# Kernel optimization log

Measured on AMD Instinct MI355X. Metric: run time of the kernel, lower is better.

## Reference

```python
import jax, jax.numpy as jnp
import numpy as np

B, S, F = 8, 4096, 512
H, A, L, DK = 8, 512, 64, 33  # n_head, n_attn, n_landmarks, d_kernel
D = A // H  # d_k = 64


def setup_inputs() -> dict:
    key = jax.random.key(0)
    ks = jax.random.split(key, 12)
    s = 0.02
    return {
        "query": jax.random.normal(ks[0], (B, S, F), jnp.float32),
        "key": jax.random.normal(ks[1], (B, S, F), jnp.float32),
        "value": jax.random.normal(ks[2], (B, S, F), jnp.float32),
        "mask": jnp.ones((B, 1, S), jnp.bool_),
        "Wq": jax.random.normal(ks[3], (F, A), jnp.float32) * s,
        "bq": jnp.zeros((A,), jnp.float32),
        "Wk": jax.random.normal(ks[4], (F, A), jnp.float32) * s,
        "bk": jnp.zeros((A,), jnp.float32),
        "Wv": jax.random.normal(ks[5], (F, A), jnp.float32) * s,
        "bv": jnp.zeros((A,), jnp.float32),
        "Wo": jax.random.normal(ks[6], (A, F), jnp.float32) * s,
        "bo": jnp.zeros((F,), jnp.float32),
        "conv_w": jax.random.normal(ks[7], (H, 1, DK, 1), jnp.float32) * s,
    }


def iterative_inv(mat, n_iter=6):
    # mat: [B, H, L, L]
    I = jnp.eye(mat.shape[-1], dtype=mat.dtype)
    K = mat
    denom = jnp.max(jnp.sum(K, axis=-2), axis=-1)[:, :, None, None]
    V = jnp.swapaxes(K, -1, -2) / denom
    for _ in range(n_iter):
        KV = K @ V
        V = 0.25 * V @ (13 * I - KV @ (15 * I - KV @ (7 * I - KV)))
    return V


def reference(query, key, value, mask, Wq, bq, Wk, bk, Wv, bv, Wo, bo, conv_w):
    nb, seq, _ = query.shape
    q = (query @ Wq + bq).reshape(nb, seq, H, D).transpose(0, 2, 1, 3)  # [B,H,S,D]
    k = (key @ Wk + bk).reshape(nb, seq, H, D).transpose(0, 2, 1, 3)
    v = (value @ Wv + bv).reshape(nb, seq, H, D).transpose(0, 2, 1, 3)
    scale = D ** -0.25
    q = q * scale
    k = k * scale
    m = seq // L + 1  # segment length per landmark
    q_rep = jnp.concatenate([q, q, q], axis=2)[:, :, : m * L, :]
    k_rep = jnp.concatenate([k, k, k], axis=2)[:, :, : m * L, :]
    q_land = q_rep.reshape(nb, H, L, m, D).mean(axis=3)  # [B,H,L,D]
    k_land = k_rep.reshape(nb, H, L, m, D).mean(axis=3)
    ker1 = jax.nn.softmax(jnp.einsum("bhsd,bhld->bhsl", q, k_land), axis=-1)
    ker2 = jax.nn.softmax(jnp.einsum("bhld,bhmd->bhlm", q_land, k_land), axis=-1)
    ker3 = jax.nn.softmax(jnp.einsum("bhld,bhsd->bhls", q_land, k), axis=-1)
    x = ker1 @ (iterative_inv(ker2) @ (ker3 @ v))  # [B,H,S,D]
    # depthwise conv over the sequence axis (kernel (DK,1), groups=H)
    pad = DK // 2
    conv_out = jax.lax.conv_general_dilated(
        v, conv_w, window_strides=(1, 1), padding=((pad, pad), (0, 0)),
        feature_group_count=H, dimension_numbers=("NCHW", "OIHW", "NCHW"))
    x = x + conv_out
    x = x.transpose(0, 2, 1, 3).reshape(nb, seq, H * D)
    return x @ Wo + bo
```

## Files before the change

kernel.cpp:

```cpp
#include <hip/hip_runtime.h>
#include <hip/hip_bf16.h>
#include <hip/hip_fp16.h>

#define SEQ 4096
#define NBATCH 8
#define NHEAD 8
#define DKW 33
#define LDP 68

typedef _Float16 f16x8 __attribute__((ext_vector_type(8)));
typedef _Float16 f16x4 __attribute__((ext_vector_type(4)));
typedef float f32x4 __attribute__((ext_vector_type(4)));

__global__ __launch_bounds__(256) void cvt_w4_k(
    const float* __restrict__ Wq, const float* __restrict__ Wk,
    const float* __restrict__ Wv, const float* __restrict__ Wo,
    _Float16* __restrict__ WtBase, float scl)
{
  __shared__ float T[64][65];
  int z = blockIdx.z;
  const float* W = (z == 0) ? Wq : (z == 1) ? Wk : (z == 2) ? Wv : Wo;
  float scale = (z < 2) ? scl : 1.0f;
  _Float16* Wt = WtBase + (size_t)z * 262144;
  int n0 = blockIdx.x * 64, k0 = blockIdx.y * 64;
  int tid = threadIdx.x;
#pragma unroll
  for (int i = 0; i < 16; i++) {
    int e = i * 256 + tid; int r = e >> 6, c = e & 63;
    T[r][c] = W[(size_t)(k0 + r) * 512 + n0 + c];
  }
  __syncthreads();
#pragma unroll
  for (int i = 0; i < 16; i++) {
    int e = i * 256 + tid; int r = e >> 6, c = e & 63;
    Wt[(size_t)(n0 + r) * 512 + k0 + c] = (_Float16)(T[c][r] * scale);
  }
}

__device__ __forceinline__ void gl_lds16(const void* g, _Float16* l) {
  __builtin_amdgcn_global_load_lds(
      (const __attribute__((address_space(1))) void*)g,
      (__attribute__((address_space(3))) void*)l, 16, 0, 0);
}

__global__ __launch_bounds__(512, 2) void gemm_bp3_k(
    const float* __restrict__ A0, const float* __restrict__ A1, const float* __restrict__ A2,
    const _Float16* __restrict__ WtBase,
    const float* __restrict__ b0, const float* __restrict__ b1, const float* __restrict__ b2,
    float scl, _Float16* __restrict__ qh, _Float16* __restrict__ kh, _Float16* __restrict__ vt)
{
  __shared__ __attribute__((aligned(16))) _Float16 Bl[128 * 516];
  const int z = blockIdx.z;
  const float* A = (z == 0) ? A0 : (z == 1) ? A1 : A2;
  const _Float16* Wt = WtBase + (size_t)z * 262144;
  const float* bias = (z == 0) ? b0 : (z == 1) ? b1 : b2;
  const float bscale = (z < 2) ? scl : 1.0f;
  const int tid = threadIdx.x;
  const int lane = tid & 63, wv = tid >> 6;
  const int l15 = lane & 15, l4 = lane >> 4;
  const int col0 = blockIdx.y * 128;
  const int row0 = blockIdx.x * 512;

  {
    int n = tid >> 2, kc = (tid & 3) * 128;
    const _Float16* wp = &Wt[(size_t)(col0 + n) * 512 + kc];
    _Float16* lp = &Bl[n * 516 + kc];
#pragma unroll
    for (int i = 0; i < 16; i++)
      *(f16x8*)&lp[i * 8] = *(const f16x8*)&wp[i * 8];
  }

  size_t abase[4];
#pragma unroll
  for (int mt = 0; mt < 4; mt++)
    abase[mt] = (size_t)(row0 + wv * 64 + mt * 16 + l15) * 512;

  auto loadA = [&](int mt, int ks) -> f16x8 {
    int k = ks * 32 + l4 * 8;
    float4 x = *(const float4*)&A[abase[mt] + k];
    float4 y = *(const float4*)&A[abase[mt] + k + 4];
    f16x8 o;
    o[0] = (_Float16)x.x; o[1] = (_Float16)x.y; o[2] = (_Float16)x.z; o[3] = (_Float16)x.w;
    o[4] = (_Float16)y.x; o[5] = (_Float16)y.y; o[6] = (_Float16)y.z; o[7] = (_Float16)y.w;
    return o;
  };

  f32x4 acc[4][8];
#pragma unroll
  for (int mt = 0; mt < 4; mt++)
#pragma unroll
    for (int n = 0; n < 8; n++) acc[mt][n] = (f32x4){0.f, 0.f, 0.f, 0.f};

  f16x8 aC[4];
#pragma unroll
  for (int mt = 0; mt < 4; mt++) aC[mt] = loadA(mt, 0);
  __syncthreads();

  for (int ks = 0; ks < 16; ks++) {
    f16x8 aN[4];
    if (ks < 15) {
#pragma unroll
      for (int mt = 0; mt < 4; mt++) aN[mt] = loadA(mt, ks + 1);
    }
    f16x8 bf[8];
#pragma unroll
    for (int n = 0; n < 8; n++)
      bf[n] = *(const f16x8*)&Bl[(n * 16 + l15) * 516 + ks * 32 + l4 * 8];
    __builtin_amdgcn_s_setprio(1);
#pragma unroll
    for (int mt = 0; mt < 4; mt++)
#pragma unroll
      for (int n = 0; n < 8; n++)
        acc[mt][n] = __builtin_amdgcn_mfma_f32_16x16x32_f16(aC[mt], bf[n], acc[mt][n], 0, 0, 0);
    __builtin_amdgcn_s_setprio(0);
    if (ks < 15) {
#pragma unroll
      for (int mt = 0; mt < 4; mt++) aC[mt] = aN[mt];
    }
  }

  float bb[8];
#pragma unroll
  for (int n = 0; n < 8; n++) bb[n] = bias[col0 + n * 16 + l15] * bscale;

  if (z == 2) {
    __syncthreads();
#pragma unroll
    for (int mt = 0; mt < 4; mt++)
#pragma unroll
      for (int n = 0; n < 8; n++) {
        f16x4 o;
#pragma unroll
        for (int r = 0; r < 4; r++) o[r] = (_Float16)(acc[mt][n][r] + bb[n]);
        *(f16x4*)&Bl[(n * 16 + l15) * 516 + wv * 64 + mt * 16 + l4 * 4] = o;
      }
    __syncthreads();
    int b = row0 >> 12, sbase = row0 & 4095;
#pragma unroll
    for (int i = 0; i < 16; i++) {
      int idx = i * 512 + tid;
      int c = idx >> 6, sc = (idx & 63) * 8;
      int colg_ = col0 + c;
      int h = colg_ >> 6, d = colg_ & 63;
      f16x8 v = *(const f16x8*)&Bl[c * 516 + sc];
      *(f16x8*)&vt[((size_t)((b * NHEAD + h) * 64 + d)) * SEQ + sbase + sc] = v;
    }
  } else {
    _Float16* outp = (z == 0) ? qh : kh;
#pragma unroll
    for (int mt = 0; mt < 4; mt++) {
      int rb = row0 + wv * 64 + mt * 16 + l4 * 4;
#pragma unroll
      for (int n = 0; n < 8; n++) {
        int col = col0 + n * 16 + l15;
        int h = col >> 6, d = col & 63;
#pragma unroll
        for (int r = 0; r < 4; r++) {
          int row = rb + r;
          int b = row >> 12, s = row & 4095;
          outp[((size_t)(b * NHEAD + h) * SEQ + s) * 64 + d] = (_Float16)(acc[mt][n][r] + bb[n]);
        }
      }
    }
  }
}

__global__ __launch_bounds__(256, 4) void gemm_gl_k(
    const _Float16* __restrict__ A, const _Float16* __restrict__ Wt,
    const float* __restrict__ bias, float* __restrict__ outp)
{
  __shared__ __attribute__((aligned(16))) _Float16 smem[16384];
  const int tid = threadIdx.x;
  const int lane = tid & 63, wv = tid >> 6;
  const int wr = wv >> 1, wc = wv & 1;
  const int l15 = lane & 15, l4 = lane >> 4;
  const int row0 = blockIdx.x * 128, col0 = blockIdx.y * 128;

  auto stage = [&](int buf, int ks) {
#pragma unroll
    for (int c = 0; c < 2; c++) {
      int u = wv * 128 + c * 64 + lane;
      int r = u & 127, s = u >> 7;
      int grow = row0 + r;
      size_t ga = ((size_t)((grow >> 12) * NHEAD + (ks >> 1)) * SEQ + (grow & 4095)) * 64
                  + (ks & 1) * 32 + s * 8;
      size_t gb = (size_t)(col0 + r) * 512 + ks * 32 + s * 8;
      int dst = (wv * 128 + c * 64) * 8;
      gl_lds16(&A[ga],  &smem[buf * 4096 + dst]);
      gl_lds16(&Wt[gb], &smem[8192 + buf * 4096 + dst]);
    }
  };

  f32x4 acc[4][4];
#pragma unroll
  for (int m = 0; m < 4; m++)
#pragma unroll
    for (int n = 0; n < 4; n++) acc[m][n] = (f32x4){0.f, 0.f, 0.f, 0.f};

  stage(0, 0);
  __syncthreads();

  for (int ks = 0; ks < 16; ks++) {
    const int cur = ks & 1;
    if (ks < 15) stage(cur ^ 1, ks + 1);
    const int ao = cur * 4096, bo = 8192 + cur * 4096;
    f16x8 af[4], bf[4];
#pragma unroll
    for (int m = 0; m < 4; m++)
      af[m] = *(const f16x8*)&smem[ao + l4 * 1024 + (wr * 64 + m * 16 + l15) * 8];
#pragma unroll
    for (int n = 0; n < 4; n++)
      bf[n] = *(const f16x8*)&smem[bo + l4 * 1024 + (wc * 64 + n * 16 + l15) * 8];
#pragma unroll
    for (int m = 0; m < 4; m++)
#pragma unroll
      for (int n = 0; n < 4; n++)
        acc[m][n] = __builtin_amdgcn_mfma_f32_16x16x32_f16(af[m], bf[n], acc[m][n], 0, 0, 0);
    __syncthreads();
  }

  float bb[4];
#pragma unroll
  for (int n = 0; n < 4; n++) bb[n] = bias[col0 + wc * 64 + n * 16 + l15];
#pragma unroll
  for (int mt = 0; mt < 4; mt++) {
    int rb = row0 + wr * 64 + mt * 16 + l4 * 4;
#pragma unroll
    for (int n = 0; n < 4; n++) {
      int col = col0 + wc * 64 + n * 16 + l15;
#pragma unroll
      for (int r = 0; r < 4; r++)
        outp[(size_t)(rb + r) * 512 + col] = acc[mt][n][r] + bb[n];
    }
  }
}

__global__ void landmarks_k(const _Float16* __restrict__ q, const _Float16* __restrict__ k,
                            float* __restrict__ qlandf, float* __restrict__ klandf,
                            _Float16* __restrict__ ql16, _Float16* __restrict__ kl16)
{
  int bhl = blockIdx.x;
  int d = threadIdx.x;
  int l = bhl & 63, bh = bhl >> 6;
  const _Float16* qp = q + (size_t)bh * SEQ * 64;
  const _Float16* kp = k + (size_t)bh * SEQ * 64;
  float sq = 0.f, sk = 0.f;
  int base = l * 65;
  for (int i = 0; i < 65; i++) {
    int s = (base + i) & 4095;
    sq += (float)qp[(size_t)s * 64 + d];
    sk += (float)kp[(size_t)s * 64 + d];
  }
  float mq = sq * (1.0f / 65.0f), mk = sk * (1.0f / 65.0f);
  qlandf[(size_t)bhl * 64 + d] = mq;
  klandf[(size_t)bhl * 64 + d] = mk;
  ql16[(size_t)bhl * 64 + d] = (_Float16)mq;
  kl16[(size_t)bhl * 64 + d] = (_Float16)mk;
}

__device__ __forceinline__ void mfma64(
    float (&C)[64][LDP], const float (&X)[64][LDP], const float (&Yt)[64][LDP],
    int wv, int l15, int l4)
{
  f16x8 ah[2], al[2];
#pragma unroll
  for (int kh = 0; kh < 2; kh++) {
    const float* xp = &X[wv * 16 + l15][kh * 32 + l4 * 8];
    float4 x0 = *(const float4*)xp;
    float4 x1 = *(const float4*)(xp + 4);
    float xv[8] = {x0.x, x0.y, x0.z, x0.w, x1.x, x1.y, x1.z, x1.w};
#pragma unroll
    for (int j = 0; j < 8; j++) {
      _Float16 h = (_Float16)xv[j];
      ah[kh][j] = h;
      al[kh][j] = (_Float16)(xv[j] - (float)h);
    }
  }
  f32x4 acc[4];
#pragma unroll
  for (int n = 0; n < 4; n++) {
    f16x8 bh_[2], bl_[2];
#pragma unroll
    for (int kh = 0; kh < 2; kh++) {
      const float* yp = &Yt[n * 16 + l15][kh * 32 + l4 * 8];
      float4 y0 = *(const float4*)yp;
      float4 y1 = *(const float4*)(yp + 4);
      float yv[8] = {y0.x, y0.y, y0.z, y0.w, y1.x, y1.y, y1.z, y1.w};
#pragma unroll
      for (int j = 0; j < 8; j++) {
        _Float16 h = (_Float16)yv[j];
        bh_[kh][j] = h;
        bl_[kh][j] = (_Float16)(yv[j] - (float)h);
      }
    }
    acc[n] = (f32x4){0.f, 0.f, 0.f, 0.f};
#pragma unroll
    for (int kh = 0; kh < 2; kh++) {
      acc[n] = __builtin_amdgcn_mfma_f32_16x16x32_f16(ah[kh], bh_[kh], acc[n], 0, 0, 0);
      acc[n] = __builtin_amdgcn_mfma_f32_16x16x32_f16(ah[kh], bl_[kh], acc[n], 0, 0, 0);
      acc[n] = __builtin_amdgcn_mfma_f32_16x16x32_f16(al[kh], bh_[kh], acc[n], 0, 0, 0);
    }
  }
#pragma unroll
  for (int n = 0; n < 4; n++)
#pragma unroll
    for (int r = 0; r < 4; r++)
      C[wv * 16 + l4 * 4 + r][n * 16 + l15] = acc[n][r];
  __syncthreads();
}

__global__ __launch_bounds__(256) void ker2_inv_k(
    const float* __restrict__ qland, const float* __restrict__ kland, float* __restrict__ invm)
{
  __shared__ float Km[64][LDP], Vm[64][LDP], VmT[64][LDP], KV[64][LDP], T1t[64][LDP], T2[64][LDP];
  __shared__ float colsum[64];
  __shared__ float denom_s;
  int bh = blockIdx.x, tid = threadIdx.x;
  int lane = tid & 63, wv = tid >> 6, l15 = lane & 15, l4 = lane >> 4;
  const float* qlp = qland + (size_t)bh * 4096;
  const float* klp = kland + (size_t)bh * 4096;
  const int r = tid >> 2, cq = (tid & 3) * 16;
#pragma unroll
  for (int j = 0; j < 4; j++) {
    *(float4*)&T2[r][cq + j * 4]  = *(const float4*)&qlp[(size_t)r * 64 + cq + j * 4];
    *(float4*)&T1t[r][cq + j * 4] = *(const float4*)&klp[(size_t)r * 64 + cq + j * 4];
  }
  __syncthreads();
  mfma64(Km, T2, T1t, wv, l15, l4);
  {
    float4 v[4];
#pragma unroll
    for (int j = 0; j < 4; j++) v[j] = *(const float4*)&Km[r][cq + j * 4];
    float mx = -1e30f;
#pragma unroll
    for (int j = 0; j < 4; j++) mx = fmaxf(mx, fmaxf(fmaxf(v[j].x, v[j].y), fmaxf(v[j].z, v[j].w)));
    mx = fmaxf(mx, __shfl_xor(mx, 1));
    mx = fmaxf(mx, __shfl_xor(mx, 2));
    float s = 0.f;
#pragma unroll
    for (int j = 0; j < 4; j++) {
      v[j].x = __expf(v[j].x - mx); v[j].y = __expf(v[j].y - mx);
      v[j].z = __expf(v[j].z - mx); v[j].w = __expf(v[j].w - mx);
      s += v[j].x + v[j].y + v[j].z + v[j].w;
    }
    s += __shfl_xor(s, 1);
    s += __shfl_xor(s, 2);
    float iv = 1.0f / s;
#pragma unroll
    for (int j = 0; j < 4; j++) {
      v[j].x *= iv; v[j].y *= iv; v[j].z *= iv; v[j].w *= iv;
      *(float4*)&Km[r][cq + j * 4] = v[j];
    }
  }
  __syncthreads();
  {
    float s = 0.f;
#pragma unroll
    for (int i = 0; i < 16; i++) s += Km[cq + i][r];
    s += __shfl_xor(s, 1);
    s += __shfl_xor(s, 2);
    if ((tid & 3) == 0) colsum[r] = s;
  }
  __syncthreads();
  if (tid < 64) {
    float v = colsum[tid];
#pragma unroll
    for (int off = 1; off < 64; off <<= 1) v = fmaxf(v, __shfl_xor(v, off));
    if (tid == 0) denom_s = v;
  }
  __syncthreads();
  {
    float dn = 1.0f / denom_s;
#pragma unroll
    for (int j = 0; j < 4; j++) {
      float4 v = *(const float4*)&Km[r][cq + j * 4];
      v.x *= dn; v.y *= dn; v.z *= dn; v.w *= dn;
      *(float4*)&VmT[r][cq + j * 4] = v;
      Vm[cq + j * 4 + 0][r] = v.x;
      Vm[cq + j * 4 + 1][r] = v.y;
      Vm[cq + j * 4 + 2][r] = v.z;
      Vm[cq + j * 4 + 3][r] = v.w;
    }
  }
  __syncthreads();
  for (int it = 0; it < 6; it++) {
    mfma64(KV, Km, VmT, wv, l15, l4);
#pragma unroll
    for (int j = 0; j < 4; j++) {
      float4 v = *(const float4*)&KV[r][cq + j * 4];
#pragma unroll
      for (int e = 0; e < 4; e++) {
        int col = cq + j * 4 + e;
        T1t[col][r] = (r == col ? 7.0f : 0.0f) - ((const float*)&v)[e];
      }
    }
    __syncthreads();
    mfma64(T2, KV, T1t, wv, l15, l4);
#pragma unroll
    for (int j = 0; j < 4; j++) {
      float4 v = *(const float4*)&T2[r][cq + j * 4];
#pragma unroll
      for (int e = 0; e < 4; e++) {
        int col = cq + j * 4 + e;
        T1t[col][r] = (r == col ? 15.0f : 0.0f) - ((const float*)&v)[e];
      }
    }
    __syncthreads();
    mfma64(T2, KV, T1t, wv, l15, l4);
#pragma unroll
    for (int j = 0; j < 4; j++) {
      float4 v = *(const float4*)&T2[r][cq + j * 4];
#pragma unroll
      for (int e = 0; e < 4; e++) {
        int col = cq + j * 4 + e;
        T1t[col][r] = (r == col ? 13.0f : 0.0f) - ((const float*)&v)[e];
      }
    }
    __syncthreads();
    mfma64(T2, Vm, T1t, wv, l15, l4);
#pragma unroll
    for (int j = 0; j < 4; j++) {
      float4 v = *(const float4*)&T2[r][cq + j * 4];
      v.x *= 0.25f; v.y *= 0.25f; v.z *= 0.25f; v.w *= 0.25f;
      *(float4*)&Vm[r][cq + j * 4] = v;
      VmT[cq + j * 4 + 0][r] = v.x;
      VmT[cq + j * 4 + 1][r] = v.y;
      VmT[cq + j * 4 + 2][r] = v.z;
      VmT[cq + j * 4 + 3][r] = v.w;
    }
    __syncthreads();
  }
#pragma unroll
  for (int j = 0; j < 4; j++)
    *(float4*)&invm[(size_t)bh * 4096 + (size_t)r * 64 + cq + j * 4] = *(const float4*)&Vm[r][cq + j * 4];
}

__global__ __launch_bounds__(256) void ker3pv_k(
    const _Float16* __restrict__ kx, const _Float16* __restrict__ vt,
    const _Float16* __restrict__ ql16,
    float* __restrict__ t1part, float* __restrict__ csumpart)
{
  __shared__ __attribute__((aligned(16))) _Float16 kls[64 * 72];
  __shared__ __attribute__((aligned(16))) _Float16 vls[64 * 72];
  __shared__ __attribute__((aligned(16))) _Float16 pls[64 * 72];
  __shared__ float red[4][64];
  int g = blockIdx.x, bh = blockIdx.y;
  int tid = threadIdx.x, lane = tid & 63, wv = tid >> 6;
  const _Float16* kp = kx + (size_t)bh * SEQ * 64;
  const _Float16* vp = vt + (size_t)bh * 64 * SEQ;
  const _Float16* qlp = ql16 + (size_t)bh * 4096;
  const int l15 = lane & 15, l4 = lane >> 4;

  f16x8 qa[4][2];
#pragma unroll
  for (int lt = 0; lt < 4; lt++)
#pragma unroll
    for (int kh = 0; kh < 2; kh++)
      qa[lt][kh] = *(const f16x8*)&qlp[(size_t)(lt * 16 + l15) * 64 + kh * 32 + l4 * 8];

  float cs[16];
#pragma unroll
  for (int i = 0; i < 16; i++) cs[i] = 0.f;
  f32x4 accp[4];
#pragma unroll
  for (int lt = 0; lt < 4; lt++) accp[lt] = (f32x4){0.f, 0.f, 0.f, 0.f};

  const int srow = tid >> 2, c4 = tid & 3;
  for (int t = 0; t < 16; t++) {
    int s0 = g * 1024 + t * 64;
    __syncthreads();
    *(f16x8*)&kls[srow * 72 + c4 * 8]       = *(const f16x8*)&kp[(size_t)(s0 + srow) * 64 + c4 * 8];
    *(f16x8*)&kls[srow * 72 + (c4 + 4) * 8] = *(const f16x8*)&kp[(size_t)(s0 + srow) * 64 + (c4 + 4) * 8];
    *(f16x8*)&vls[srow * 72 + c4 * 8]       = *(const f16x8*)&vp[(size_t)srow * SEQ + s0 + c4 * 8];
    *(f16x8*)&vls[srow * 72 + (c4 + 4) * 8] = *(const f16x8*)&vp[(size_t)srow * SEQ + s0 + (c4 + 4) * 8];
    __syncthreads();
    f16x8 kb[2];
    kb[0] = *(const f16x8*)&kls[(wv * 16 + l15) * 72 + l4 * 8];
    kb[1] = *(const f16x8*)&kls[(wv * 16 + l15) * 72 + 32 + l4 * 8];
    f32x4 C[4];
#pragma unroll
    for (int lt = 0; lt < 4; lt++) {
      C[lt] = (f32x4){0.f, 0.f, 0.f, 0.f};
      C[lt] = __builtin_amdgcn_mfma_f32_16x16x32_f16(qa[lt][0], kb[0], C[lt], 0, 0, 0);
      C[lt] = __builtin_amdgcn_mfma_f32_16x16x32_f16(qa[lt][1], kb[1], C[lt], 0, 0, 0);
    }
#pragma unroll
    for (int lt = 0; lt < 4; lt++)
#pragma unroll
      for (int r = 0; r < 4; r++) {
        float e = __expf(C[lt][r]);
        cs[lt * 4 + r] += e;
        pls[(lt * 16 + l4 * 4 + r) * 72 + wv * 16 + l15] = (_Float16)e;
      }
    __syncthreads();
    f16x8 va[2];
    va[0] = *(const f16x8*)&vls[(wv * 16 + l15) * 72 + l4 * 8];
    va[1] = *(const f16x8*)&vls[(wv * 16 + l15) * 72 + 32 + l4 * 8];
#pragma unroll
    for (int lt = 0; lt < 4; lt++) {
      f16x8 pb0 = *(const f16x8*)&pls[(lt * 16 + l15) * 72 + l4 * 8];
      f16x8 pb1 = *(const f16x8*)&pls[(lt * 16 + l15) * 72 + 32 + l4 * 8];
      accp[lt] = __builtin_amdgcn_mfma_f32_16x16x32_f16(va[0], pb0, accp[lt], 0, 0, 0);
      accp[lt] = __builtin_amdgcn_mfma_f32_16x16x32_f16(va[1], pb1, accp[lt], 0, 0, 0);
    }
  }
  size_t pbase = ((size_t)(bh * 4 + g)) * 4096;
#pragma unroll
  for (int lt = 0; lt < 4; lt++)
#pragma unroll
    for (int r = 0; r < 4; r++)
      t1part[pbase + (size_t)(wv * 16 + l4 * 4 + r) * 64 + lt * 16 + l15] = accp[lt][r];
#pragma unroll
  for (int i = 0; i < 16; i++) {
    cs[i] += __shfl_xor(cs[i], 1);
    cs[i] += __shfl_xor(cs[i], 2);
    cs[i] += __shfl_xor(cs[i], 4);
    cs[i] += __shfl_xor(cs[i], 8);
  }
  if (l15 == 0) {
#pragma unroll
    for (int lt = 0; lt < 4; lt++)
#pragma unroll
      for (int r = 0; r < 4; r++)
        red[wv][lt * 16 + l4 * 4 + r] = cs[lt * 4 + r];
  }
  __syncthreads();
  if (tid < 64)
    csumpart[((size_t)(bh * 4 + g)) * 64 + tid] = red[0][tid] + red[1][tid] + red[2][tid] + red[3][tid];
}

__global__ void t1_reduce_k(const float* __restrict__ t1part, const float* __restrict__ csumpart,
                            float* __restrict__ t1r)
{
  int i = blockIdx.x * 256 + threadIdx.x;
  int bh = i >> 12, dl = i & 4095, l = dl & 63;
  float s = 0.f, cssum = 0.f;
#pragma unroll
  for (int g = 0; g < 4; g++) {
    s += t1part[(((size_t)(bh * 4 + g)) << 12) + dl];
    cssum += csumpart[(((size_t)(bh * 4 + g)) << 6) + l];
  }
  t1r[i] = s / cssum;
}

__global__ __launch_bounds__(256) void t2_mm_k(
    const float* __restrict__ invm, const float* __restrict__ t1r, _Float16* __restrict__ t2t)
{
  __shared__ float T[64][68];
  __shared__ float I[64][68];
  int bh = blockIdx.x;
  int tid = threadIdx.x;
  const float* ip = invm + (size_t)bh * 4096;
  const float* tp = t1r + (size_t)bh * 4096;
  int r = tid >> 2;
#pragma unroll
  for (int mq = 0; mq < 4; mq++) {
    int d0 = (tid & 3) * 16 + mq * 4;
    *(float4*)&T[r][d0] = *(const float4*)&tp[(size_t)r * 64 + d0];
    *(float4*)&I[r][d0] = *(const float4*)&ip[(size_t)r * 64 + d0];
  }
  __syncthreads();
  int ty = tid >> 4, tx = tid & 15;
  float acc[4][4] = {};
#pragma unroll 4
  for (int kk = 0; kk < 64; kk++) {
    float a_[4], b_[4];
#pragma unroll
    for (int i = 0; i < 4; i++) a_[i] = T[ty * 4 + i][kk];
#pragma unroll
    for (int j = 0; j < 4; j++) b_[j] = I[tx * 4 + j][kk];
#pragma unroll
    for (int i = 0; i < 4; i++)
#pragma unroll
      for (int j = 0; j < 4; j++)
        acc[i][j] = fmaf(a_[i], b_[j], acc[i][j]);
  }
#pragma unroll
  for (int i = 0; i < 4; i++) {
    f16x4 o;
    o[0] = (_Float16)acc[i][0]; o[1] = (_Float16)acc[i][1];
    o[2] = (_Float16)acc[i][2]; o[3] = (_Float16)acc[i][3];
    *(f16x4*)&t2t[(size_t)bh * 4096 + (size_t)(ty * 4 + i) * 64 + tx * 4] = o;
  }
}

__global__ __launch_bounds__(256) void x1conv_k(
    const _Float16* __restrict__ qx, const _Float16* __restrict__ kl16,
    const _Float16* __restrict__ t2t, const _Float16* __restrict__ vt,
    const float* __restrict__ cw, _Float16* __restrict__ xq)
{
  __shared__ __attribute__((aligned(16))) _Float16 qls[64 * 72];
  __shared__ __attribute__((aligned(16))) _Float16 t2ls[64 * 72];
  __shared__ __attribute__((aligned(16))) _Float16 pls[64 * 72];
  __shared__ __attribute__((aligned(16))) _Float16 vls[64 * 98];
  int c = blockIdx.x, bh = blockIdx.y;
  int s0 = c * 64;
  int tid = threadIdx.x, lane = tid & 63, wv = tid >> 6;
  const int l15 = lane & 15, l4 = lane >> 4;
  const int h = bh & 7;
  const _Float16* qp = qx + ((size_t)bh * SEQ + s0) * 64;
  const int srow = tid >> 2, c4 = tid & 3;
  *(f16x8*)&qls[srow * 72 + c4 * 8]       = *(const f16x8*)&qp[(size_t)srow * 64 + c4 * 8];
  *(f16x8*)&qls[srow * 72 + (c4 + 4) * 8] = *(const f16x8*)&qp[(size_t)srow * 64 + (c4 + 4) * 8];
  *(f16x8*)&t2ls[srow * 72 + c4 * 8]       = *(const f16x8*)&t2t[(size_t)bh * 4096 + (size_t)srow * 64 + c4 * 8];
  *(f16x8*)&t2ls[srow * 72 + (c4 + 4) * 8] = *(const f16x8*)&t2t[(size_t)bh * 4096 + (size_t)srow * 64 + (c4 + 4) * 8];
  {
    const _Float16* vp = vt + ((size_t)bh * 64 + srow) * SEQ;
    int base = s0 - 16 + c4 * 24;
#pragma unroll
    for (int i = 0; i < 3; i++) {
      int s = base + i * 8;
      f16x8 v;
      if (s >= 0 && s + 8 <= SEQ) {
        v = *(const f16x8*)&vp[s];
      } else {
#pragma unroll
        for (int j = 0; j < 8; j++) {
          int sj = s + j;
          v[j] = (sj >= 0 && sj < SEQ) ? vp[sj] : (_Float16)0.f;
        }
      }
      *(f16x8*)&vls[srow * 98 + c4 * 24 + i * 8] = v;
    }
  }
  float w[DKW];
#pragma unroll
  for (int j = 0; j < DKW; j++) w[j] = cw[h * DKW + j];
  f16x8 klb[4][2];
#pragma unroll
  for (int lt = 0; lt < 4; lt++)
#pragma unroll
    for (int kh = 0; kh < 2; kh++)
      klb[lt][kh] = *(const f16x8*)&kl16[(size_t)bh * 4096 + (size_t)(lt * 16 + l15) * 64 + kh * 32 + l4 * 8];
  __syncthreads();
  f16x8 qaf[2];
  qaf[0] = *(const f16x8*)&qls[(wv * 16 + l15) * 72 + l4 * 8];
  qaf[1] = *(const f16x8*)&qls[(wv * 16 + l15) * 72 + 32 + l4 * 8];
  f32x4 C[4];
#pragma unroll
  for (int lt = 0; lt < 4; lt++) {
    C[lt] = (f32x4){0.f, 0.f, 0.f, 0.f};
    C[lt] = __builtin_amdgcn_mfma_f32_16x16x32_f16(qaf[0], klb[lt][0], C[lt], 0, 0, 0);
    C[lt] = __builtin_amdgcn_mfma_f32_16x16x32_f16(qaf[1], klb[lt][1], C[lt], 0, 0, 0);
  }
  float e[16], rs[4];
#pragma unroll
  for (int r = 0; r < 4; r++) rs[r] = 0.f;
#pragma unroll
  for (int lt = 0; lt < 4; lt++)
#pragma unroll
    for (int r = 0; r < 4; r++) {
      e[lt * 4 + r] = __expf(C[lt][r]);
      rs[r] += e[lt * 4 + r];
    }
#pragma unroll
  for (int r = 0; r < 4; r++) {
    rs[r] += __shfl_xor(rs[r], 1);
    rs[r] += __shfl_xor(rs[r], 2);
    rs[r] += __shfl_xor(rs[r], 4);
    rs[r] += __shfl_xor(rs[r], 8);
    rs[r] = 1.0f / rs[r];
  }
#pragma unroll
  for (int lt = 0; lt < 4; lt++)
#pragma unroll
    for (int r = 0; r < 4; r++)
      pls[(wv * 16 + l4 * 4 + r) * 72 + lt * 16 + l15] = (_Float16)(e[lt * 4 + r] * rs[r]);
  __syncthreads();
  f16x8 pa[2];
  pa[0] = *(const f16x8*)&pls[(wv * 16 + l15) * 72 + l4 * 8];
  pa[1] = *(const f16x8*)&pls[(wv * 16 + l15) * 72 + 32 + l4 * 8];
  __syncthreads();
  {
    int d = tid & 63, sg = tid >> 6;
    float win[48];
#pragma unroll
    for (int t = 0; t < 48; t++) win[t] = (float)vls[d * 98 + sg * 16 + t];
#pragma unroll
    for (int i = 0; i < 16; i++) {
      float a = 0.f;
#pragma unroll
      for (int j = 0; j < DKW; j++) a = fmaf(w[j], win[i + j], a);
      pls[(sg * 16 + i) * 72 + d] = (_Float16)a;
    }
  }
  __syncthreads();
#pragma unroll
  for (int dt = 0; dt < 4; dt++) {
    f16x8 tb0 = *(const f16x8*)&t2ls[(dt * 16 + l15) * 72 + l4 * 8];
    f16x8 tb1 = *(const f16x8*)&t2ls[(dt * 16 + l15) * 72 + 32 + l4 * 8];
    f32x4 X = (f32x4){0.f, 0.f, 0.f, 0.f};
    X = __builtin_amdgcn_mfma_f32_16x16x32_f16(pa[0], tb0, X, 0, 0, 0);
    X = __builtin_amdgcn_mfma_f32_16x16x32_f16(pa[1], tb1, X, 0, 0, 0);
#pragma unroll
    for (int r = 0; r < 4; r++) {
      int sl = wv * 16 + l4 * 4 + r;
      int d = dt * 16 + l15;
      float vvv = X[r] + (float)pls[sl * 72 + d];
      xq[((size_t)bh * SEQ + s0 + sl) * 64 + d] = (_Float16)vvv;
    }
  }
}

extern "C" void kernel_launch(void* const* d_in, const int* in_sizes, int n_in,
                              void* d_out, int out_size, void* d_ws, size_t ws_size,
                              hipStream_t stream)
{
  (void)in_sizes; (void)n_in; (void)out_size; (void)ws_size;
  const float* query = (const float*)d_in[0];
  const float* key_  = (const float*)d_in[1];
  const float* value = (const float*)d_in[2];
  const float* Wq = (const float*)d_in[4];
  const float* bq = (const float*)d_in[5];
  const float* Wk = (const float*)d_in[6];
  const float* bk = (const float*)d_in[7];
  const float* Wv = (const float*)d_in[8];
  const float* bv = (const float*)d_in[9];
  const float* Wo = (const float*)d_in[10];
  const float* bo = (const float*)d_in[11];
  const float* cw = (const float*)d_in[12];
  float* out = (float*)d_out;

  const size_t NQ = (size_t)NBATCH * NHEAD * SEQ * 64;
  _Float16* qh  = (_Float16*)d_ws;
  _Float16* kh  = qh + NQ;
  _Float16* vt  = kh + NQ;
  _Float16* WtB = vt + NQ;
  _Float16* WoT = WtB + 3 * 262144;
  _Float16* ql16 = WtB + 4 * 262144;
  _Float16* kl16 = ql16 + 262144;
  _Float16* t2t  = kl16 + 262144;
  float* qlandf = (float*)(t2t + 262144);
  float* klandf = qlandf + 262144;
  float* invb   = klandf + 262144;
  float* t1r    = invb + 262144;
  float* t1part = t1r + 262144;
  float* csumpart = t1part + 4 * 262144;

  const float scl = 0.3535533905932738f;

  cvt_w4_k<<<dim3(8, 8, 4), 256, 0, stream>>>(Wq, Wk, Wv, Wo, WtB, scl);

  gemm_bp3_k<<<dim3(64, 4, 3), 512, 0, stream>>>(query, key_, value, WtB,
                                                 bq, bk, bv, scl, qh, kh, vt);

  landmarks_k<<<4096, 64, 0, stream>>>(qh, kh, qlandf, klandf, ql16, kl16);
  ker2_inv_k<<<64, 256, 0, stream>>>(qlandf, klandf, invb);
  ker3pv_k<<<dim3(4, 64), 256, 0, stream>>>(kh, vt, ql16, t1part, csumpart);
  t1_reduce_k<<<1024, 256, 0, stream>>>(t1part, csumpart, t1r);
  t2_mm_k<<<64, 256, 0, stream>>>(invb, t1r, t2t);
  x1conv_k<<<dim3(64, 64), 256, 0, stream>>>(qh, kl16, t2t, vt, cw, qh);
  gemm_gl_k<<<dim3(256, 4), 256, 0, stream>>>(qh, WoT, bo, out);
}
```

Measured before the change: 295.1 us.

## Merge iterative inverse and ker3·V into one launch, fold reduction into t2

Combines the independent ker2 iterative-inverse kernel (64 blocks) and the ker3·V partial kernel (256 blocks) into one 320-block launch. Blocks pick their role from the block index and share one static shared-memory buffer. The separate t1 reduce kernel is removed, and t2_mm_k now sums the four partials and applies the column-sum normalization itself. The aim is to cut two launches and let the serial inverse run alongside the streaming work. The cost is that every block reserves about 104 KB of shared memory, which can limit how many ker3 blocks are resident per CU.

Result: faster. 273.3 us (-7.4%).

```diff
diff --git a/kernel.cpp b/kernel.cpp
--- a/kernel.cpp
+++ b/kernel.cpp
@@ -259,7 +259,7 @@
 }
 
 __device__ __forceinline__ void mfma64(
-    float (&C)[64][LDP], const float (&X)[64][LDP], const float (&Yt)[64][LDP],
+    float (*C)[LDP], const float (*X)[LDP], const float (*Yt)[LDP],
     int wv, int l15, int l4)
 {
   f16x8 ah[2], al[2];
@@ -309,254 +309,264 @@
   __syncthreads();
 }
 
-__global__ __launch_bounds__(256) void ker2_inv_k(
-    const float* __restrict__ qland, const float* __restrict__ kland, float* __restrict__ invm)
-{
-  __shared__ float Km[64][LDP], Vm[64][LDP], VmT[64][LDP], KV[64][LDP], T1t[64][LDP], T2[64][LDP];
-  __shared__ float colsum[64];
-  __shared__ float denom_s;
-  int bh = blockIdx.x, tid = threadIdx.x;
-  int lane = tid & 63, wv = tid >> 6, l15 = lane & 15, l4 = lane >> 4;
-  const float* qlp = qland + (size_t)bh * 4096;
-  const float* klp = kland + (size_t)bh * 4096;
-  const int r = tid >> 2, cq = (tid & 3) * 16;
-#pragma unroll
-  for (int j = 0; j < 4; j++) {
-    *(float4*)&T2[r][cq + j * 4]  = *(const float4*)&qlp[(size_t)r * 64 + cq + j * 4];
-    *(float4*)&T1t[r][cq + j * 4] = *(const float4*)&klp[(size_t)r * 64 + cq + j * 4];
-  }
-  __syncthreads();
-  mfma64(Km, T2, T1t, wv, l15, l4);
-  {
-    float4 v[4];
-#pragma unroll
-    for (int j = 0; j < 4; j++) v[j] = *(const float4*)&Km[r][cq + j * 4];
-    float mx = -1e30f;
-#pragma unroll
-    for (int j = 0; j < 4; j++) mx = fmaxf(mx, fmaxf(fmaxf(v[j].x, v[j].y), fmaxf(v[j].z, v[j].w)));
-    mx = fmaxf(mx, __shfl_xor(mx, 1));
-    mx = fmaxf(mx, __shfl_xor(mx, 2));
-    float s = 0.f;
-#pragma unroll
-    for (int j = 0; j < 4; j++) {
-      v[j].x = __expf(v[j].x - mx); v[j].y = __expf(v[j].y - mx);
-      v[j].z = __expf(v[j].z - mx); v[j].w = __expf(v[j].w - mx);
-      s += v[j].x + v[j].y + v[j].z + v[j].w;
-    }
-    s += __shfl_xor(s, 1);
-    s += __shfl_xor(s, 2);
-    float iv = 1.0f / s;
-#pragma unroll
-    for (int j = 0; j < 4; j++) {
-      v[j].x *= iv; v[j].y *= iv; v[j].z *= iv; v[j].w *= iv;
-      *(float4*)&Km[r][cq + j * 4] = v[j];
-    }
-  }
-  __syncthreads();
-  {
-    float s = 0.f;
-#pragma unroll
-    for (int i = 0; i < 16; i++) s += Km[cq + i][r];
-    s += __shfl_xor(s, 1);
-    s += __shfl_xor(s, 2);
-    if ((tid & 3) == 0) colsum[r] = s;
-  }
-  __syncthreads();
-  if (tid < 64) {
-    float v = colsum[tid];
-#pragma unroll
-    for (int off = 1; off < 64; off <<= 1) v = fmaxf(v, __shfl_xor(v, off));
-    if (tid == 0) denom_s = v;
-  }
-  __syncthreads();
-  {
-    float dn = 1.0f / denom_s;
-#pragma unroll
-    for (int j = 0; j < 4; j++) {
-      float4 v = *(const float4*)&Km[r][cq + j * 4];
-      v.x *= dn; v.y *= dn; v.z *= dn; v.w *= dn;
-      *(float4*)&VmT[r][cq + j * 4] = v;
-      Vm[cq + j * 4 + 0][r] = v.x;
-      Vm[cq + j * 4 + 1][r] = v.y;
-      Vm[cq + j * 4 + 2][r] = v.z;
-      Vm[cq + j * 4 + 3][r] = v.w;
-    }
-  }
-  __syncthreads();
-  for (int it = 0; it < 6; it++) {
-    mfma64(KV, Km, VmT, wv, l15, l4);
-#pragma unroll
-    for (int j = 0; j < 4; j++) {
-      float4 v = *(const float4*)&KV[r][cq + j * 4];
-#pragma unroll
-      for (int e = 0; e < 4; e++) {
-        int col = cq + j * 4 + e;
-        T1t[col][r] = (r == col ? 7.0f : 0.0f) - ((const float*)&v)[e];
-      }
-    }
-    __syncthreads();
-    mfma64(T2, KV, T1t, wv, l15, l4);
-#pragma unroll
-    for (int j = 0; j < 4; j++) {
-      float4 v = *(const float4*)&T2[r][cq + j * 4];
-#pragma unroll
-      for (int e = 0; e < 4; e++) {
-        int col = cq + j * 4 + e;
-        T1t[col][r] = (r == col ? 15.0f : 0.0f) - ((const float*)&v)[e];
-      }
-    }
-    __syncthreads();
-    mfma64(T2, KV, T1t, wv, l15, l4);
-#pragma unroll
-    for (int j = 0; j < 4; j++) {
-      float4 v = *(const float4*)&T2[r][cq + j * 4];
-#pragma unroll
-      for (int e = 0; e < 4; e++) {
-        int col = cq + j * 4 + e;
-        T1t[col][r] = (r == col ? 13.0f : 0.0f) - ((const float*)&v)[e];
-      }
-    }
-    __syncthreads();
-    mfma64(T2, Vm, T1t, wv, l15, l4);
-#pragma unroll
-    for (int j = 0; j < 4; j++) {
-      float4 v = *(const float4*)&T2[r][cq + j * 4];
-      v.x *= 0.25f; v.y *= 0.25f; v.z *= 0.25f; v.w *= 0.25f;
-      *(float4*)&Vm[r][cq + j * 4] = v;
-      VmT[cq + j * 4 + 0][r] = v.x;
-      VmT[cq + j * 4 + 1][r] = v.y;
-      VmT[cq + j * 4 + 2][r] = v.z;
-      VmT[cq + j * 4 + 3][r] = v.w;
-    }
-    __syncthreads();
-  }
-#pragma unroll
-  for (int j = 0; j < 4; j++)
-    *(float4*)&invm[(size_t)bh * 4096 + (size_t)r * 64 + cq + j * 4] = *(const float4*)&Vm[r][cq + j * 4];
-}
-
-__global__ __launch_bounds__(256) void ker3pv_k(
+#define SMEM_BYTES 104712
+
+__global__ __launch_bounds__(256) void attn_mid_k(
+    const float* __restrict__ qland, const float* __restrict__ kland,
     const _Float16* __restrict__ kx, const _Float16* __restrict__ vt,
     const _Float16* __restrict__ ql16,
-    float* __restrict__ t1part, float* __restrict__ csumpart)
-{
-  __shared__ __attribute__((aligned(16))) _Float16 kls[64 * 72];
-  __shared__ __attribute__((aligned(16))) _Float16 vls[64 * 72];
-  __shared__ __attribute__((aligned(16))) _Float16 pls[64 * 72];
-  __shared__ float red[4][64];
-  int g = blockIdx.x, bh = blockIdx.y;
-  int tid = threadIdx.x, lane = tid & 63, wv = tid >> 6;
-  const _Float16* kp = kx + (size_t)bh * SEQ * 64;
-  const _Float16* vp = vt + (size_t)bh * 64 * SEQ;
-  const _Float16* qlp = ql16 + (size_t)bh * 4096;
+    float* __restrict__ invm, float* __restrict__ t1part, float* __restrict__ csumpart)
+{
+  __shared__ __attribute__((aligned(16))) char smem[SMEM_BYTES];
+  const int bid = blockIdx.x;
+  const int tid = threadIdx.x;
+  const int lane = tid & 63, wv = tid >> 6;
   const int l15 = lane & 15, l4 = lane >> 4;
 
-  f16x8 qa[4][2];
-#pragma unroll
-  for (int lt = 0; lt < 4; lt++)
-#pragma unroll
-    for (int kh = 0; kh < 2; kh++)
-      qa[lt][kh] = *(const f16x8*)&qlp[(size_t)(lt * 16 + l15) * 64 + kh * 32 + l4 * 8];
-
-  float cs[16];
-#pragma unroll
-  for (int i = 0; i < 16; i++) cs[i] = 0.f;
-  f32x4 accp[4];
-#pragma unroll
-  for (int lt = 0; lt < 4; lt++) accp[lt] = (f32x4){0.f, 0.f, 0.f, 0.f};
-
-  const int srow = tid >> 2, c4 = tid & 3;
-  for (int t = 0; t < 16; t++) {
-    int s0 = g * 1024 + t * 64;
-    __syncthreads();
-    *(f16x8*)&kls[srow * 72 + c4 * 8]       = *(const f16x8*)&kp[(size_t)(s0 + srow) * 64 + c4 * 8];
-    *(f16x8*)&kls[srow * 72 + (c4 + 4) * 8] = *(const f16x8*)&kp[(size_t)(s0 + srow) * 64 + (c4 + 4) * 8];
-    *(f16x8*)&vls[srow * 72 + c4 * 8]       = *(const f16x8*)&vp[(size_t)srow * SEQ + s0 + c4 * 8];
-    *(f16x8*)&vls[srow * 72 + (c4 + 4) * 8] = *(const f16x8*)&vp[(size_t)srow * SEQ + s0 + (c4 + 4) * 8];
-    __syncthreads();
-    f16x8 kb[2];
-    kb[0] = *(const f16x8*)&kls[(wv * 16 + l15) * 72 + l4 * 8];
-    kb[1] = *(const f16x8*)&kls[(wv * 16 + l15) * 72 + 32 + l4 * 8];
-    f32x4 C[4];
-#pragma unroll
-    for (int lt = 0; lt < 4; lt++) {
-      C[lt] = (f32x4){0.f, 0.f, 0.f, 0.f};
-      C[lt] = __builtin_amdgcn_mfma_f32_16x16x32_f16(qa[lt][0], kb[0], C[lt], 0, 0, 0);
-      C[lt] = __builtin_amdgcn_mfma_f32_16x16x32_f16(qa[lt][1], kb[1], C[lt], 0, 0, 0);
-    }
+  if (bid < 64) {
+    float (*Km)[LDP]  = (float (*)[LDP])(smem);
+    float (*Vm)[LDP]  = (float (*)[LDP])(smem + 17408);
+    float (*VmT)[LDP] = (float (*)[LDP])(smem + 2 * 17408);
+    float (*KV)[LDP]  = (float (*)[LDP])(smem + 3 * 17408);
+    float (*T1t)[LDP] = (float (*)[LDP])(smem + 4 * 17408);
+    float (*T2)[LDP]  = (float (*)[LDP])(smem + 5 * 17408);
+    float* colsum = (float*)(smem + 6 * 17408);
+    const int bh = bid;
+    const float* qlp = qland + (size_t)bh * 4096;
+    const float* klp = kland + (size_t)bh * 4096;
+    const int r = tid >> 2, cq = (tid & 3) * 16;
+#pragma unroll
+    for (int j = 0; j < 4; j++) {
+      *(float4*)&T2[r][cq + j * 4]  = *(const float4*)&qlp[(size_t)r * 64 + cq + j * 4];
+      *(float4*)&T1t[r][cq + j * 4] = *(const float4*)&klp[(size_t)r * 64 + cq + j * 4];
+    }
+    __syncthreads();
+    mfma64(Km, T2, T1t, wv, l15, l4);
+    {
+      float4 v[4];
+#pragma unroll
+      for (int j = 0; j < 4; j++) v[j] = *(const float4*)&Km[r][cq + j * 4];
+      float mx = -1e30f;
+#pragma unroll
+      for (int j = 0; j < 4; j++) mx = fmaxf(mx, fmaxf(fmaxf(v[j].x, v[j].y), fmaxf(v[j].z, v[j].w)));
+      mx = fmaxf(mx, __shfl_xor(mx, 1));
+      mx = fmaxf(mx, __shfl_xor(mx, 2));
+      float s = 0.f;
+#pragma unroll
+      for (int j = 0; j < 4; j++) {
+        v[j].x = __expf(v[j].x - mx); v[j].y = __expf(v[j].y - mx);
+        v[j].z = __expf(v[j].z - mx); v[j].w = __expf(v[j].w - mx);
+        s += v[j].x + v[j].y + v[j].z + v[j].w;
+      }
+      s += __shfl_xor(s, 1);
+      s += __shfl_xor(s, 2);
+      float iv = 1.0f / s;
+#pragma unroll
+      for (int j = 0; j < 4; j++) {
+        v[j].x *= iv; v[j].y *= iv; v[j].z *= iv; v[j].w *= iv;
+        *(float4*)&Km[r][cq + j * 4] = v[j];
+      }
+    }
+    __syncthreads();
+    {
+      float s = 0.f;
+#pragma unroll
+      for (int i = 0; i < 16; i++) s += Km[cq + i][r];
+      s += __shfl_xor(s, 1);
+      s += __shfl_xor(s, 2);
+      if ((tid & 3) == 0) colsum[r] = s;
+    }
+    __syncthreads();
+    if (tid < 64) {
+      float v = colsum[tid];
+#pragma unroll
+      for (int off = 1; off < 64; off <<= 1) v = fmaxf(v, __shfl_xor(v, off));
+      if (tid == 0) colsum[64] = v;
+    }
+    __syncthreads();
+    {
+      float dn = 1.0f / colsum[64];
+#pragma unroll
+      for (int j = 0; j < 4; j++) {
+        float4 v = *(const float4*)&Km[r][cq + j * 4];
+        v.x *= dn; v.y *= dn; v.z *= dn; v.w *= dn;
+        *(float4*)&VmT[r][cq + j * 4] = v;
+        Vm[cq + j * 4 + 0][r] = v.x;
+        Vm[cq + j * 4 + 1][r] = v.y;
+        Vm[cq + j * 4 + 2][r] = v.z;
+        Vm[cq + j * 4 + 3][r] = v.w;
+      }
+    }
+    __syncthreads();
+    for (int it = 0; it < 6; it++) {
+      mfma64(KV, Km, VmT, wv, l15, l4);
+#pragma unroll
+      for (int j = 0; j < 4; j++) {
+        float4 v = *(const float4*)&KV[r][cq + j * 4];
+#pragma unroll
+        for (int e = 0; e < 4; e++) {
+          int col = cq + j * 4 + e;
+          T1t[col][r] = (r == col ? 7.0f : 0.0f) - ((const float*)&v)[e];
+        }
+      }
+      __syncthreads();
+      mfma64(T2, KV, T1t, wv, l15, l4);
+#pragma unroll
+      for (int j = 0; j < 4; j++) {
+        float4 v = *(const float4*)&T2[r][cq + j * 4];
+#pragma unroll
+        for (int e = 0; e < 4; e++) {
+          int col = cq + j * 4 + e;
+          T1t[col][r] = (r == col ? 15.0f : 0.0f) - ((const float*)&v)[e];
+        }
+      }
+      __syncthreads();
+      mfma64(T2, KV, T1t, wv, l15, l4);
+#pragma unroll
+      for (int j = 0; j < 4; j++) {
+        float4 v = *(const float4*)&T2[r][cq + j * 4];
+#pragma unroll
+        for (int e = 0; e < 4; e++) {
+          int col = cq + j * 4 + e;
+          T1t[col][r] = (r == col ? 13.0f : 0.0f) - ((const float*)&v)[e];
+        }
+      }
+      __syncthreads();
+      mfma64(T2, Vm, T1t, wv, l15, l4);
+#pragma unroll
+      for (int j = 0; j < 4; j++) {
+        float4 v = *(const float4*)&T2[r][cq + j * 4];
+        v.x *= 0.25f; v.y *= 0.25f; v.z *= 0.25f; v.w *= 0.25f;
+        *(float4*)&Vm[r][cq + j * 4] = v;
+        VmT[cq + j * 4 + 0][r] = v.x;
+        VmT[cq + j * 4 + 1][r] = v.y;
+        VmT[cq + j * 4 + 2][r] = v.z;
+        VmT[cq + j * 4 + 3][r] = v.w;
+      }
+      __syncthreads();
+    }
+#pragma unroll
+    for (int j = 0; j < 4; j++)
+      *(float4*)&invm[(size_t)bh * 4096 + (size_t)r * 64 + cq + j * 4] = *(const float4*)&Vm[r][cq + j * 4];
+  } else {
+    _Float16* kls = (_Float16*)smem;
+    _Float16* vls = kls + 64 * 72;
+    _Float16* pls = vls + 64 * 72;
+    float (*red)[64] = (float (*)[64])(pls + 64 * 72);
+    const int idx = bid - 64;
+    const int g = idx & 3, bh = idx >> 2;
+    const _Float16* kp = kx + (size_t)bh * SEQ * 64;
+    const _Float16* vp = vt + (size_t)bh * 64 * SEQ;
+    const _Float16* qlp = ql16 + (size_t)bh * 4096;
+
+    f16x8 qa[4][2];
 #pragma unroll
     for (int lt = 0; lt < 4; lt++)
 #pragma unroll
-      for (int r = 0; r < 4; r++) {
-        float e = __expf(C[lt][r]);
-        cs[lt * 4 + r] += e;
-        pls[(lt * 16 + l4 * 4 + r) * 72 + wv * 16 + l15] = (_Float16)e;
-      }
-    __syncthreads();
-    f16x8 va[2];
-    va[0] = *(const f16x8*)&vls[(wv * 16 + l15) * 72 + l4 * 8];
-    va[1] = *(const f16x8*)&vls[(wv * 16 + l15) * 72 + 32 + l4 * 8];
-#pragma unroll
-    for (int lt = 0; lt < 4; lt++) {
-      f16x8 pb0 = *(const f16x8*)&pls[(lt * 16 + l15) * 72 + l4 * 8];
-      f16x8 pb1 = *(const f16x8*)&pls[(lt * 16 + l15) * 72 + 32 + l4 * 8];
-      accp[lt] = __builtin_amdgcn_mfma_f32_16x16x32_f16(va[0], pb0, accp[lt], 0, 0, 0);
-      accp[lt] = __builtin_amdgcn_mfma_f32_16x16x32_f16(va[1], pb1, accp[lt], 0, 0, 0);
-    }
-  }
-  size_t pbase = ((size_t)(bh * 4 + g)) * 4096;
-#pragma unroll
-  for (int lt = 0; lt < 4; lt++)
-#pragma unroll
-    for (int r = 0; r < 4; r++)
-      t1part[pbase + (size_t)(wv * 16 + l4 * 4 + r) * 64 + lt * 16 + l15] = accp[lt][r];
-#pragma unroll
-  for (int i = 0; i < 16; i++) {
-    cs[i] += __shfl_xor(cs[i], 1);
-    cs[i] += __shfl_xor(cs[i], 2);
-    cs[i] += __shfl_xor(cs[i], 4);
-    cs[i] += __shfl_xor(cs[i], 8);
-  }
-  if (l15 == 0) {
+      for (int kh = 0; kh < 2; kh++)
+        qa[lt][kh] = *(const f16x8*)&qlp[(size_t)(lt * 16 + l15) * 64 + kh * 32 + l4 * 8];
+
+    float cs[16];
+#pragma unroll
+    for (int i = 0; i < 16; i++) cs[i] = 0.f;
+    f32x4 accp[4];
+#pragma unroll
+    for (int lt = 0; lt < 4; lt++) accp[lt] = (f32x4){0.f, 0.f, 0.f, 0.f};
+
+    const int srow = tid >> 2, c4 = tid & 3;
+    for (int t = 0; t < 16; t++) {
+      int s0 = g * 1024 + t * 64;
+      __syncthreads();
+      *(f16x8*)&kls[srow * 72 + c4 * 8]       = *(const f16x8*)&kp[(size_t)(s0 + srow) * 64 + c4 * 8];
+      *(f16x8*)&kls[srow * 72 + (c4 + 4) * 8] = *(const f16x8*)&kp[(size_t)(s0 + srow) * 64 + (c4 + 4) * 8];
+      *(f16x8*)&vls[srow * 72 + c4 * 8]       = *(const f16x8*)&vp[(size_t)srow * SEQ + s0 + c4 * 8];
+      *(f16x8*)&vls[srow * 72 + (c4 + 4) * 8] = *(const f16x8*)&vp[(size_t)srow * SEQ + s0 + (c4 + 4) * 8];
+      __syncthreads();
+      f16x8 kb[2];
+      kb[0] = *(const f16x8*)&kls[(wv * 16 + l15) * 72 + l4 * 8];
+      kb[1] = *(const f16x8*)&kls[(wv * 16 + l15) * 72 + 32 + l4 * 8];
+      f32x4 C[4];
+#pragma unroll
+      for (int lt = 0; lt < 4; lt++) {
+        C[lt] = (f32x4){0.f, 0.f, 0.f, 0.f};
+        C[lt] = __builtin_amdgcn_mfma_f32_16x16x32_f16(qa[lt][0], kb[0], C[lt], 0, 0, 0);
+        C[lt] = __builtin_amdgcn_mfma_f32_16x16x32_f16(qa[lt][1], kb[1], C[lt], 0, 0, 0);
+      }
+#pragma unroll
+      for (int lt = 0; lt < 4; lt++)
+#pragma unroll
+        for (int r = 0; r < 4; r++) {
+          float e = __expf(C[lt][r]);
+          cs[lt * 4 + r] += e;
+          pls[(lt * 16 + l4 * 4 + r) * 72 + wv * 16 + l15] = (_Float16)e;
+        }
+      __syncthreads();
+      f16x8 va[2];
+      va[0] = *(const f16x8*)&vls[(wv * 16 + l15) * 72 + l4 * 8];
+      va[1] = *(const f16x8*)&vls[(wv * 16 + l15) * 72 + 32 + l4 * 8];
+#pragma unroll
+      for (int lt = 0; lt < 4; lt++) {
+        f16x8 pb0 = *(const f16x8*)&pls[(lt * 16 + l15) * 72 + l4 * 8];
+        f16x8 pb1 = *(const f16x8*)&pls[(lt * 16 + l15) * 72 + 32 + l4 * 8];
+        accp[lt] = __builtin_amdgcn_mfma_f32_16x16x32_f16(va[0], pb0, accp[lt], 0, 0, 0);
+        accp[lt] = __builtin_amdgcn_mfma_f32_16x16x32_f16(va[1], pb1, accp[lt], 0, 0, 0);
+      }
+    }
+    size_t pbase = ((size_t)(bh * 4 + g)) * 4096;
 #pragma unroll
     for (int lt = 0; lt < 4; lt++)
 #pragma unroll
       for (int r = 0; r < 4; r++)
-        red[wv][lt * 16 + l4 * 4 + r] = cs[lt * 4 + r];
-  }
-  __syncthreads();
-  if (tid < 64)
-    csumpart[((size_t)(bh * 4 + g)) * 64 + tid] = red[0][tid] + red[1][tid] + red[2][tid] + red[3][tid];
-}
-
-__global__ void t1_reduce_k(const float* __restrict__ t1part, const float* __restrict__ csumpart,
-                            float* __restrict__ t1r)
-{
-  int i = blockIdx.x * 256 + threadIdx.x;
-  int bh = i >> 12, dl = i & 4095, l = dl & 63;
-  float s = 0.f, cssum = 0.f;
-#pragma unroll
-  for (int g = 0; g < 4; g++) {
-    s += t1part[(((size_t)(bh * 4 + g)) << 12) + dl];
-    cssum += csumpart[(((size_t)(bh * 4 + g)) << 6) + l];
-  }
-  t1r[i] = s / cssum;
+        t1part[pbase + (size_t)(wv * 16 + l4 * 4 + r) * 64 + lt * 16 + l15] = accp[lt][r];
+#pragma unroll
+    for (int i = 0; i < 16; i++) {
+      cs[i] += __shfl_xor(cs[i], 1);
+      cs[i] += __shfl_xor(cs[i], 2);
+      cs[i] += __shfl_xor(cs[i], 4);
+      cs[i] += __shfl_xor(cs[i], 8);
+    }
+    if (l15 == 0) {
+#pragma unroll
+      for (int lt = 0; lt < 4; lt++)
+#pragma unroll
+        for (int r = 0; r < 4; r++)
+          red[wv][lt * 16 + l4 * 4 + r] = cs[lt * 4 + r];
+    }
+    __syncthreads();
+    if (tid < 64)
+      csumpart[((size_t)(bh * 4 + g)) * 64 + tid] = red[0][tid] + red[1][tid] + red[2][tid] + red[3][tid];
+  }
 }
 
 __global__ __launch_bounds__(256) void t2_mm_k(
-    const float* __restrict__ invm, const float* __restrict__ t1r, _Float16* __restrict__ t2t)
+    const float* __restrict__ invm, const float* __restrict__ t1part,
+    const float* __restrict__ csumpart, _Float16* __restrict__ t2t)
 {
   __shared__ float T[64][68];
   __shared__ float I[64][68];
+  __shared__ float csum[64];
   int bh = blockIdx.x;
   int tid = threadIdx.x;
   const float* ip = invm + (size_t)bh * 4096;
-  const float* tp = t1r + (size_t)bh * 4096;
+  if (tid < 64) {
+    float s = 0.f;
+#pragma unroll
+    for (int g = 0; g < 4; g++) s += csumpart[(((size_t)(bh * 4 + g)) << 6) + tid];
+    csum[tid] = 1.0f / s;
+  }
+  __syncthreads();
   int r = tid >> 2;
 #pragma unroll
   for (int mq = 0; mq < 4; mq++) {
     int d0 = (tid & 3) * 16 + mq * 4;
-    *(float4*)&T[r][d0] = *(const float4*)&tp[(size_t)r * 64 + d0];
+    float4 s = {0.f, 0.f, 0.f, 0.f};
+#pragma unroll
+    for (int g = 0; g < 4; g++) {
+      float4 v = *(const float4*)&t1part[(((size_t)(bh * 4 + g)) << 12) + (size_t)r * 64 + d0];
+      s.x += v.x; s.y += v.y; s.z += v.z; s.w += v.w;
+    }
+    s.x *= csum[d0 + 0]; s.y *= csum[d0 + 1]; s.z *= csum[d0 + 2]; s.w *= csum[d0 + 3];
+    *(float4*)&T[r][d0] = s;
     *(float4*)&I[r][d0] = *(const float4*)&ip[(size_t)r * 64 + d0];
   }
   __syncthreads();
@@ -745,10 +755,9 @@
                                                  bq, bk, bv, scl, qh, kh, vt);
 
   landmarks_k<<<4096, 64, 0, stream>>>(qh, kh, qlandf, klandf, ql16, kl16);
-  ker2_inv_k<<<64, 256, 0, stream>>>(qlandf, klandf, invb);
-  ker3pv_k<<<dim3(4, 64), 256, 0, stream>>>(kh, vt, ql16, t1part, csumpart);
-  t1_reduce_k<<<1024, 256, 0, stream>>>(t1part, csumpart, t1r);
-  t2_mm_k<<<64, 256, 0, stream>>>(invb, t1r, t2t);
+  attn_mid_k<<<320, 256, 0, stream>>>(qlandf, klandf, kh, vt, ql16,
+                                      invb, t1part, csumpart);
+  t2_mm_k<<<64, 256, 0, stream>>>(invb, t1part, csumpart, t2t);
   x1conv_k<<<dim3(64, 64), 256, 0, stream>>>(qh, kl16, t2t, vt, cw, qh);
   gemm_gl_k<<<dim3(256, 4), 256, 0, stream>>>(qh, WoT, bo, out);
 }
```
